# Performance work log

Measured on AMD Instinct MI355X. Metric: run time of the kernel, lower is better.

## Reference

```python
import jax, jax.numpy as jnp
import numpy as np

# (pt, eta, phi) feature indices per particle for each block (eta=None for MET)
A_PT, A_ETA, A_PHI = [5, 4, 35, 34], [9, 8, 45, 44], [13, 12, 55, 54]            # e3,e2,j9,j8
B_PT, B_ETA, B_PHI = [3, 33, 31, 2], [7, 43, 41, 6], [11, 53, 51, 10]            # e1,j7,j5,e0
C_PT, C_ETA, C_PHI = [28, 32, 15, 16], [38, 42, 19, 20], [48, 52, 23, 24]        # j2,j6,mu1,mu2
D_PT, D_ETA, D_PHI = [0, 14, 30, 26, 29, 27, 17], [None, 18, 40, 36, 39, 37, 21], [1, 22, 50, 46, 49, 47, 25]  # MET,mu0,j4,j0,j3,j1,mu3


def _bc(a, nd):
    # broadcast a (B,) or () angle factor over nd trailing qubit axes
    return a.reshape(a.shape + (1,) * nd)


def _rx(state, theta, w):
    nd = state.ndim - 2
    c = _bc(jnp.cos(theta * 0.5), nd)
    s = _bc(jnp.sin(theta * 0.5), nd)
    s0 = jnp.take(state, 0, axis=w + 1)
    s1 = jnp.take(state, 1, axis=w + 1)
    return jnp.stack([c * s0 - 1j * s * s1, -1j * s * s0 + c * s1], axis=w + 1)


def _ry(state, theta, w):
    nd = state.ndim - 2
    c = _bc(jnp.cos(theta * 0.5), nd)
    s = _bc(jnp.sin(theta * 0.5), nd)
    s0 = jnp.take(state, 0, axis=w + 1)
    s1 = jnp.take(state, 1, axis=w + 1)
    return jnp.stack([c * s0 - s * s1, s * s0 + c * s1], axis=w + 1)


def _rz(state, theta, w):
    nd = state.ndim - 2
    ph = _bc(jnp.exp(-0.5j * theta.astype(state.dtype)), nd)
    s0 = jnp.take(state, 0, axis=w + 1)
    s1 = jnp.take(state, 1, axis=w + 1)
    return jnp.stack([ph * s0, jnp.conj(ph) * s1], axis=w + 1)


def _cnot(state, ctrl, tgt):
    c0 = jnp.take(state, 0, axis=ctrl + 1)
    c1 = jnp.take(state, 1, axis=ctrl + 1)
    t_ax = tgt + 1 if tgt < ctrl else tgt  # ctrl axis removed shifts higher wires down
    c1 = jnp.flip(c1, axis=t_ax)
    return jnp.stack([c0, c1], axis=ctrl + 1)


def _extract(x, pt_idx, eta_idx, phi_idx):
    pt = x[:, np.array(pt_idx)]
    eta = jnp.stack([x[:, i] if i is not None else jnp.zeros(x.shape[0], x.dtype) for i in eta_idx], axis=1)
    phi = x[:, np.array(phi_idx)]
    return pt, eta, phi


def _run_block(pt, eta, phi, weights, n, latent, trash, depth):
    B = pt.shape[0]
    state = jnp.zeros((B,) + (2,) * n, dtype=jnp.complex64)
    state = state.at[(slice(None),) + (0,) * n].set(1.0)
    for k in range(n):
        state = _rx(state, eta[:, k], k)
        state = _ry(state, pt[:, k], k)
        state = _rz(state, phi[:, k], k)
    for k in range(n - 1):
        state = _cnot(state, k, k + 1)
    for k in range(n):
        state = _rz(state, eta[:, k], k)
        state = _ry(state, pt[:, k], k)
        state = _rx(state, phi[:, k], k)
    for d in range(depth):
        for t in trash:
            for l in latent:
                state = _cnot(state, t, l)
        for k in range(n):
            state = _ry(state, weights[d * n + k], k)
        for l in latent:
            for t in trash:
                state = _cnot(state, l, t)
    p = jnp.abs(state) ** 2  # (B, 2,...,2) real probabilities
    red = tuple(range(1, n))
    zs = [jnp.sum(jnp.take(p, 0, axis=w + 1), axis=red) - jnp.sum(jnp.take(p, 1, axis=w + 1), axis=red) for w in trash]
    return jnp.stack(zs, axis=1)


def setup_inputs() -> dict:
    key = jax.random.key(0)
    k0, k1, k2, k3, k4 = jax.random.split(key, 5)
    B = 131072
    x = jax.random.normal(k0, (B, 56), dtype=jnp.float32)
    wA = 0.01 * jax.random.normal(k1, (4,), dtype=jnp.float32)
    wB = 0.01 * jax.random.normal(k2, (4,), dtype=jnp.float32)
    wC = 0.01 * jax.random.normal(k3, (4,), dtype=jnp.float32)
    wD = 0.01 * jax.random.normal(k4, (28,), dtype=jnp.float32)
    return {"x": x, "wA": wA, "wB": wB, "wC": wC, "wD": wD}


def reference(x, wA, wB, wC, wD):
    zA = _run_block(*_extract(x, A_PT, A_ETA, A_PHI), wA, 4, (0, 1), (2, 3), 1)  # (B,2)
    zB = _run_block(*_extract(x, B_PT, B_ETA, B_PHI), wB, 4, (0, 1), (2, 3), 1)  # (B,2)
    zC = _run_block(*_extract(x, C_PT, C_ETA, C_PHI), wC, 4, (0, 1), (2, 3), 1)  # (B,2)
    zD = _run_block(*_extract(x, D_PT, D_ETA, D_PHI), wD, 7, (0, 1, 2, 3), (4, 5, 6), 4)  # (B,3)
    return jnp.concatenate([zA, zB, zC, zD], axis=1)  # (B,9) ~ dict values concatenated
```

## Files before the change

kernel.cpp:

```cpp
#include <hip/hip_runtime.h>
#include <hip/hip_fp16.h>


#define DEVINL __device__ __forceinline__

typedef _Float16 hv2 __attribute__((ext_vector_type(2)));
typedef unsigned int u32;
typedef u32 vreg16 __attribute__((ext_vector_type(16)));
typedef u32 vreg64 __attribute__((ext_vector_type(64)));

struct C2 { __half2 rr, mp; };

DEVINL C2 mkc(float re, float im) {
  C2 c; c.rr = __floats2half2_rn(re, re); c.mp = __floats2half2_rn(-im, im); return c;
}
DEVINL __half2 mkamp(float re, float im) { return __floats2half2_rn(re, im); }
DEVINL __half2 swap2(__half2 v) { return __lowhigh2highlow(v); }
DEVINL __half2 cmulc(C2 u, __half2 v) { return __hfma2(u.rr, v, __hmul2(u.mp, swap2(v))); }

DEVINL float ampsq(__half2 v, float acc) {
#if __has_builtin(__builtin_amdgcn_fdot2)
  return __builtin_amdgcn_fdot2(__builtin_bit_cast(hv2, v), __builtin_bit_cast(hv2, v), acc, false);
#else
  float2 f = __half22float2(v);
  return fmaf(f.x, f.x, fmaf(f.y, f.y, acc));
#endif
}

constexpr int parc(int x) { x ^= x >> 4; x ^= x >> 2; x ^= x >> 1; return x & 1; }

struct c32 { float x, y; };
DEVINL c32 cmulf(c32 a, c32 b) { return { a.x*b.x - a.y*b.y, a.x*b.y + a.y*b.x }; }

template<class VT>
DEVINL __half2 vget(const VT& A, int i) { return __builtin_bit_cast(__half2, (u32)A[i]); }
template<class VT>
DEVINL void vset(VT& A, int i, __half2 v) { A[i] = __builtin_bit_cast(u32, v); }

DEVINL __half2 lx1(__half2 v) {
  int q = __shfl_xor(__builtin_bit_cast(int, v), 1, 64);
  return __builtin_bit_cast(__half2, q);
}
DEVINL float lx1f(float v) { return __shfl_xor(v, 1, 64); }


template<int N, int W, class VT>
DEVINL void g_ry(VT& A, __half2 c2, __half2 s2, __half2 ns2) {
  constexpr int M = 1 << (N - 1 - W);
#pragma unroll
  for (int i = 0; i < (1 << N); ++i) if (!(i & M)) {
    const int j = i | M;
    __half2 v0 = vget(A, i), v1 = vget(A, j);
    vset(A, i, __hfma2(c2, v0, __hmul2(ns2, v1)));
    vset(A, j, __hfma2(c2, v1, __hmul2(s2, v0)));
  }
}

template<int N, int W, class VT>
DEVINL void g_u2(VT& A, C2 u00, C2 u01, C2 u10, C2 u11) {
  constexpr int M = 1 << (N - 1 - W);
#pragma unroll
  for (int i = 0; i < (1 << N); ++i) if (!(i & M)) {
    const int j = i | M;
    __half2 v0 = vget(A, i), v1 = vget(A, j), v0s = swap2(v0), v1s = swap2(v1);
    vset(A, i, __hfma2(u00.rr, v0, __hfma2(u00.mp, v0s, __hfma2(u01.rr, v1, __hmul2(u01.mp, v1s)))));
    vset(A, j, __hfma2(u10.rr, v0, __hfma2(u10.mp, v0s, __hfma2(u11.rr, v1, __hmul2(u11.mp, v1s)))));
  }
}

template<int N, int C, int T, class VT>
DEVINL void g_cnot(VT& A) {
  constexpr int CM = 1 << (N - 1 - C), TM = 1 << (N - 1 - T);
#pragma unroll
  for (int i = 0; i < (1 << N); ++i) if ((i & CM) && !(i & TM)) {
    const int j = i | TM;
    __half2 t = vget(A, i); vset(A, i, vget(A, j)); vset(A, j, t);
  }
}

template<int N, int K, class VT>
DEVINL void chain_cnot(VT& A) {
  if constexpr (K < N - 1) { g_cnot<N, K, K + 1>(A); chain_cnot<N, K + 1>(A); }
}


DEVINL void mk_u01(float ce, float se, float cp, float sp, float cf, float sf,
                   c32& u0, c32& u1) {
  u0 = cmulf({cf, -sf}, {cp * ce, sp * se});
  u1 = cmulf({cf,  sf}, {sp * ce, -cp * se});
}

DEVINL void mk_U(float ce, float se, float cp, float sp, float cf, float sf,
                 C2& U00, C2& U01, C2& U10, C2& U11) {
  c32 z = {ce, -se}, zb = {ce, se};
  c32 A = cmulf({cf * cp, -sf * sp}, z);
  c32 T = cmulf({cf * sp,  sf * cp}, zb);
  c32 Cc = cmulf({cf * sp, -sf * cp}, z);
  c32 D = cmulf({cf * cp,  sf * sp}, zb);
  U00 = mkc(A.x, A.y); U01 = mkc(-T.x, -T.y); U10 = mkc(Cc.x, Cc.y); U11 = mkc(D.x, D.y);
}

DEVINL void load_sc(const float* __restrict__ xr, int eta_i, int pt_i, int phi_i,
                    float& ce, float& se, float& cp, float& sp, float& cf, float& sf) {
  float e = (eta_i < 0) ? 0.f : xr[eta_i];
  __sincosf(0.5f * e, &se, &ce);
  __sincosf(0.5f * xr[pt_i], &sp, &cp);
  __sincosf(0.5f * xr[phi_i], &sf, &cf);
}

template<int N, int M, class VT, class CF>
DEVINL void build_rec(VT& A, CF cf) {
  if constexpr (M < N) {
    c32 u0, u1; cf(M, u0, u1);
    C2 c0 = mkc(u0.x, u0.y), c1 = mkc(u1.x, u1.y);
#pragma unroll
    for (int j = (1 << M) - 1; j >= 0; --j) {
      __half2 s = vget(A, j);
      vset(A, 2 * j,     cmulc(c0, s));
      vset(A, 2 * j + 1, cmulc(c1, s));
    }
    build_rec<N, M + 1>(A, cf);
  }
}

template<int N, int K, class VT, class CF>
DEVINL void usweep_rec(VT& A, CF cf) {
  if constexpr (K < N) {
    C2 U00, U01, U10, U11;
    cf(K, U00, U01, U10, U11);
    g_u2<N, K>(A, U00, U01, U10, U11);
    usweep_rec<N, K + 1>(A, cf);
  }
}

template<int N, int K, class VT, class CF>
DEVINL void ry_rec(VT& A, CF cf) {
  if constexpr (K < N) {
    __half2 c2, s2, ns2;
    cf(K, c2, s2, ns2);
    g_ry<N, K>(A, c2, s2, ns2);
    ry_rec<N, K + 1>(A, cf);
  }
}


template<int I>
DEVINL void sim4h(const float* __restrict__ xr, const float* __restrict__ w, float* z) {
  constexpr int PT[3][4]  = {{5, 4, 35, 34}, {3, 33, 31, 2}, {28, 32, 15, 16}};
  constexpr int ETA[3][4] = {{9, 8, 45, 44}, {7, 43, 41, 6}, {38, 42, 19, 20}};
  constexpr int PHI[3][4] = {{13, 12, 55, 54}, {11, 53, 51, 10}, {48, 52, 23, 24}};
  vreg16 A;
  vset(A, 0, mkamp(1.f, 0.f));
  build_rec<4, 0>(A, [&](int M, c32& u0, c32& u1) {
    float ce, se, cp, sp, cf, sf;
    load_sc(xr, ETA[I][M], PT[I][M], PHI[I][M], ce, se, cp, sp, cf, sf);
    mk_u01(ce, se, cp, sp, cf, sf, u0, u1);
  });
  chain_cnot<4, 0>(A);
  usweep_rec<4, 0>(A, [&](int K, C2& U00, C2& U01, C2& U10, C2& U11) {
    float ce, se, cp, sp, cf, sf;
    load_sc(xr, ETA[I][K], PT[I][K], PHI[I][K], ce, se, cp, sp, cf, sf);
    mk_U(ce, se, cp, sp, cf, sf, U00, U01, U10, U11);
  });

#pragma unroll
  for (int i = 0; i < 16; ++i)
    if (parc(i & 3) && !(i & 8)) {
      __half2 t = vget(A, i); vset(A, i, vget(A, i ^ 12)); vset(A, i ^ 12, t);
    }

  ry_rec<4, 0>(A, [&](int K, __half2& c2, __half2& s2, __half2& ns2) {
    float sv, cv; __sincosf(0.5f * w[K], &sv, &cv);
    c2 = __floats2half2_rn(cv, cv);
    s2 = __floats2half2_rn(sv, sv);
    ns2 = __floats2half2_rn(-sv, -sv);
  });

#pragma unroll
  for (int i = 0; i < 16; ++i)
    if (parc(i & 12) && !(i & 2)) {
      __half2 t = vget(A, i); vset(A, i, vget(A, i ^ 3)); vset(A, i ^ 3, t);
    }

  float cls[4];
#pragma unroll
  for (int c = 0; c < 4; ++c) cls[c] = 0.f;
#pragma unroll
  for (int i = 0; i < 16; ++i) cls[i & 3] = ampsq(vget(A, i), cls[i & 3]);
  float z0 = 0.f, z1 = 0.f;
#pragma unroll
  for (int c = 0; c < 4; ++c) {
    z0 += (c & 2) ? -cls[c] : cls[c];
    z1 += (c & 1) ? -cls[c] : cls[c];
  }
  z[0] = z0; z[1] = z1;
}


DEVINL void role7(const float* __restrict__ xr, const float* __restrict__ wD,
                  float* __restrict__ out_row, bool po) {
  constexpr int PT[7]  = {0, 14, 30, 26, 29, 27, 17};
  constexpr int ETA[7] = {-1, 18, 40, 36, 39, 37, 21};
  constexpr int PHI[7] = {1, 22, 50, 46, 49, 47, 25};

  vreg64 A;
  vset(A, 0, mkamp(1.f, 0.f));
  build_rec<6, 0>(A, [&](int M, c32& u0, c32& u1) {
    const int k = M + 1;
    float ce, se, cp, sp, cf, sf;
    load_sc(xr, ETA[k], PT[k], PHI[k], ce, se, cp, sp, cf, sf);
    mk_u01(ce, se, cp, sp, cf, sf, u0, u1);
  });
  {
    float ce, se, cp, sp, cf, sf;
    load_sc(xr, ETA[0], PT[0], PHI[0], ce, se, cp, sp, cf, sf);
    c32 u0, u1; mk_u01(ce, se, cp, sp, cf, sf, u0, u1);
    C2 c0 = mkc(po ? u1.x : u0.x, po ? u1.y : u0.y);
#pragma unroll
    for (int i = 0; i < 64; ++i) vset(A, i, cmulc(c0, vget(A, i)));
  }

#pragma unroll
  for (int i = 0; i < 32; ++i) {
    const int j = i | 32;
    __half2 lo = vget(A, i), hi = vget(A, j);
    vset(A, i, po ? hi : lo);
    vset(A, j, po ? lo : hi);
  }
  chain_cnot<6, 0>(A);

  {
    float ce, se, cp, sp, cf, sf;
    load_sc(xr, ETA[0], PT[0], PHI[0], ce, se, cp, sp, cf, sf);
    C2 U00, U01, U10, U11;
    mk_U(ce, se, cp, sp, cf, sf, U00, U01, U10, U11);
    C2 UA, UB;
    UA.rr = po ? U11.rr : U00.rr; UA.mp = po ? U11.mp : U00.mp;
    UB.rr = po ? U10.rr : U01.rr; UB.mp = po ? U10.mp : U01.mp;
#pragma unroll
    for (int i = 0; i < 64; ++i) {
      __half2 m = vget(A, i), q = lx1(m);
      vset(A, i, __hfma2(UA.rr, m, __hfma2(UA.mp, swap2(m),
                 __hfma2(UB.rr, q, __hmul2(UB.mp, swap2(q))))));
    }
  }
  usweep_rec<6, 0>(A, [&](int W, C2& U00, C2& U01, C2& U10, C2& U11) {
    const int k = W + 1;
    float ce, se, cp, sp, cf, sf;
    load_sc(xr, ETA[k], PT[k], PHI[k], ce, se, cp, sp, cf, sf);
    mk_U(ce, se, cp, sp, cf, sf, U00, U01, U10, U11);
  });

#pragma unroll 1
  for (int d = 0; d < 4; ++d) {
#pragma unroll
    for (int i = 0; i < 64; ++i)
      if (parc(i & 7) && !(i & 0x20)) {
        const int j = i ^ 0x38;
        __half2 t0 = lx1(vget(A, j));
        __half2 t1 = lx1(vget(A, i));
        vset(A, i, t0); vset(A, j, t1);
      }

    {
      float sv, cv; __sincosf(0.5f * wD[7 * d], &sv, &cv);
      __half2 c2v = __floats2half2_rn(cv, cv);
      __half2 sp2 = __floats2half2_rn(po ? sv : -sv, po ? sv : -sv);
#pragma unroll
      for (int i = 0; i < 64; ++i) {
        __half2 q = lx1(vget(A, i));
        vset(A, i, __hfma2(c2v, vget(A, i), __hmul2(sp2, q)));
      }
    }
    ry_rec<6, 0>(A, [&](int W, __half2& c2, __half2& s2, __half2& ns2) {
      float sv, cv; __sincosf(0.5f * wD[7 * d + W + 1], &sv, &cv);
      c2 = __floats2half2_rn(cv, cv);
      s2 = __floats2half2_rn(sv, sv);
      ns2 = __floats2half2_rn(-sv, -sv);
    });

#pragma unroll
    for (int i = 0; i < 64; ++i)
      if (!(i & 4)) {
        const int j = i ^ 7;
        const bool cond = parc(i & 0x38) ? !po : po;
        __half2 lo = vget(A, i), hi = vget(A, j);
        vset(A, i, cond ? hi : lo);
        vset(A, j, cond ? lo : hi);
      }
  }

  float cls[8];
#pragma unroll
  for (int c = 0; c < 8; ++c) cls[c] = 0.f;
#pragma unroll
  for (int i = 0; i < 64; ++i) cls[i & 7] = ampsq(vget(A, i), cls[i & 7]);
  float z4 = 0.f, z5 = 0.f, z6 = 0.f;
#pragma unroll
  for (int c = 0; c < 8; ++c) {
    z4 += (c & 4) ? -cls[c] : cls[c];
    z5 += (c & 2) ? -cls[c] : cls[c];
    z6 += (c & 1) ? -cls[c] : cls[c];
  }
  z4 += lx1f(z4); z5 += lx1f(z5); z6 += lx1f(z6);
  if (!po) {
    out_row[6] = z4; out_row[7] = z5; out_row[8] = z6;
  }
}


__global__ void __launch_bounds__(256, 2)
k_all(const float* __restrict__ x,
      const float* __restrict__ wA, const float* __restrict__ wB,
      const float* __restrict__ wC, const float* __restrict__ wD,
      float* __restrict__ out, int B, int gx) {
  const int bx = blockIdx.x;
  if (bx < gx) {
    const int b = bx * 256 + threadIdx.x;
    if (b >= B) return;
    const float* xr = x + (size_t)b * 56;
    float o[6];
    sim4h<0>(xr, wA, &o[0]);
    sim4h<1>(xr, wB, &o[2]);
    sim4h<2>(xr, wC, &o[4]);
    float* op = out + (size_t)b * 9;
#pragma unroll
    for (int i = 0; i < 6; ++i) op[i] = o[i];
  } else {
    const int t = (bx - gx) * 256 + threadIdx.x;
    const int b = t >> 1;
    if (b >= B) return;
    const bool po = (t & 1) != 0;
    role7(x + (size_t)b * 56, wD, out + (size_t)b * 9, po);
  }
}


extern "C" void kernel_launch(void* const* d_in, const int* in_sizes, int n_in,
                              void* d_out, int out_size, void* d_ws, size_t ws_size,
                              hipStream_t stream) {
  const float* x  = (const float*)d_in[0];
  const float* wA = (const float*)d_in[1];
  const float* wB = (const float*)d_in[2];
  const float* wC = (const float*)d_in[3];
  const float* wD = (const float*)d_in[4];
  float* out = (float*)d_out;
  const int B = in_sizes[0] / 56;
  const int threads = 256;

  const int gx = (B + threads - 1) / threads;
  const int gy = (2 * B + threads - 1) / threads;
  k_all<<<gx + gy, threads, 0, stream>>>(x, wA, wB, wC, wD, out, B, gx);
}
```

Measured before the change: 138.4 us.

## Split 7-qubit block state across four lanes instead of two

The 7-qubit simulation now distributes the 128-amplitude state over four lanes (32 half2 registers each) rather than two lanes with 64 registers. Gates on the top two qubits become cross-lane shuffles with xor 1, 2 or 3, and the CNOT permutations are rewritten for the new lane mapping. The launch-bounds occupancy hint rises from 2 to 8 to use the lower register pressure. The cost is twice as many threads for this block, more shuffles per gate, redundant per-lane angle computation, and an extra shuffle-reduction step at the end.

```diff
diff --git a/kernel.cpp b/kernel.cpp
--- a/kernel.cpp
+++ b/kernel.cpp
@@ -7,7 +7,7 @@
 typedef _Float16 hv2 __attribute__((ext_vector_type(2)));
 typedef unsigned int u32;
 typedef u32 vreg16 __attribute__((ext_vector_type(16)));
-typedef u32 vreg64 __attribute__((ext_vector_type(64)));
+typedef u32 vreg32 __attribute__((ext_vector_type(32)));
 
 struct C2 { __half2 rr, mp; };
 
@@ -37,11 +37,13 @@
 template<class VT>
 DEVINL void vset(VT& A, int i, __half2 v) { A[i] = __builtin_bit_cast(u32, v); }
 
-DEVINL __half2 lx1(__half2 v) {
-  int q = __shfl_xor(__builtin_bit_cast(int, v), 1, 64);
+template<int K>
+DEVINL __half2 lxk(__half2 v) {
+  int q = __shfl_xor(__builtin_bit_cast(int, v), K, 64);
   return __builtin_bit_cast(__half2, q);
 }
-DEVINL float lx1f(float v) { return __shfl_xor(v, 1, 64); }
+template<int K>
+DEVINL float lxkf(float v) { return __shfl_xor(v, K, 64); }
 
 
 template<int N, int W, class VT>
@@ -198,15 +200,18 @@
 
 
 DEVINL void role7(const float* __restrict__ xr, const float* __restrict__ wD,
-                  float* __restrict__ out_row, bool po) {
+                  float* __restrict__ out_row, int sub) {
+  const bool b0 = (sub & 2) != 0;
+  const bool b1 = (sub & 1) != 0;
+
   constexpr int PT[7]  = {0, 14, 30, 26, 29, 27, 17};
   constexpr int ETA[7] = {-1, 18, 40, 36, 39, 37, 21};
   constexpr int PHI[7] = {1, 22, 50, 46, 49, 47, 25};
 
-  vreg64 A;
+  vreg32 A;
   vset(A, 0, mkamp(1.f, 0.f));
-  build_rec<6, 0>(A, [&](int M, c32& u0, c32& u1) {
-    const int k = M + 1;
+  build_rec<5, 0>(A, [&](int M, c32& u0, c32& u1) {
+    const int k = M + 2;
     float ce, se, cp, sp, cf, sf;
     load_sc(xr, ETA[k], PT[k], PHI[k], ce, se, cp, sp, cf, sf);
     mk_u01(ce, se, cp, sp, cf, sf, u0, u1);
@@ -214,20 +219,30 @@
   {
     float ce, se, cp, sp, cf, sf;
     load_sc(xr, ETA[0], PT[0], PHI[0], ce, se, cp, sp, cf, sf);
-    c32 u0, u1; mk_u01(ce, se, cp, sp, cf, sf, u0, u1);
-    C2 c0 = mkc(po ? u1.x : u0.x, po ? u1.y : u0.y);
-#pragma unroll
-    for (int i = 0; i < 64; ++i) vset(A, i, cmulc(c0, vget(A, i)));
+    c32 q0u0, q0u1; mk_u01(ce, se, cp, sp, cf, sf, q0u0, q0u1);
+    load_sc(xr, ETA[1], PT[1], PHI[1], ce, se, cp, sp, cf, sf);
+    c32 q1u0, q1u1; mk_u01(ce, se, cp, sp, cf, sf, q1u0, q1u1);
+    c32 f0 = b0 ? q0u1 : q0u0;
+    c32 f1 = b1 ? q1u1 : q1u0;
+    c32 f = cmulf(f0, f1);
+    C2 cf2 = mkc(f.x, f.y);
+#pragma unroll
+    for (int i = 0; i < 32; ++i) vset(A, i, cmulc(cf2, vget(A, i)));
   }
 
 #pragma unroll
   for (int i = 0; i < 32; ++i) {
-    const int j = i | 32;
+    __half2 q = lxk<1>(vget(A, i));
+    if (true) vset(A, i, b0 ? q : vget(A, i));
+  }
+#pragma unroll
+  for (int i = 0; i < 16; ++i) {
+    const int j = i | 16;
     __half2 lo = vget(A, i), hi = vget(A, j);
-    vset(A, i, po ? hi : lo);
-    vset(A, j, po ? lo : hi);
-  }
-  chain_cnot<6, 0>(A);
+    vset(A, i, b1 ? hi : lo);
+    vset(A, j, b1 ? lo : hi);
+  }
+  chain_cnot<5, 0>(A);
 
   {
     float ce, se, cp, sp, cf, sf;
@@ -235,17 +250,32 @@
     C2 U00, U01, U10, U11;
     mk_U(ce, se, cp, sp, cf, sf, U00, U01, U10, U11);
     C2 UA, UB;
-    UA.rr = po ? U11.rr : U00.rr; UA.mp = po ? U11.mp : U00.mp;
-    UB.rr = po ? U10.rr : U01.rr; UB.mp = po ? U10.mp : U01.mp;
-#pragma unroll
-    for (int i = 0; i < 64; ++i) {
-      __half2 m = vget(A, i), q = lx1(m);
+    UA.rr = b0 ? U11.rr : U00.rr; UA.mp = b0 ? U11.mp : U00.mp;
+    UB.rr = b0 ? U10.rr : U01.rr; UB.mp = b0 ? U10.mp : U01.mp;
+#pragma unroll
+    for (int i = 0; i < 32; ++i) {
+      __half2 m = vget(A, i), q = lxk<2>(m);
       vset(A, i, __hfma2(UA.rr, m, __hfma2(UA.mp, swap2(m),
                  __hfma2(UB.rr, q, __hmul2(UB.mp, swap2(q))))));
     }
   }
-  usweep_rec<6, 0>(A, [&](int W, C2& U00, C2& U01, C2& U10, C2& U11) {
-    const int k = W + 1;
+  {
+    float ce, se, cp, sp, cf, sf;
+    load_sc(xr, ETA[1], PT[1], PHI[1], ce, se, cp, sp, cf, sf);
+    C2 U00, U01, U10, U11;
+    mk_U(ce, se, cp, sp, cf, sf, U00, U01, U10, U11);
+    C2 UA, UB;
+    UA.rr = b1 ? U11.rr : U00.rr; UA.mp = b1 ? U11.mp : U00.mp;
+    UB.rr = b1 ? U10.rr : U01.rr; UB.mp = b1 ? U10.mp : U01.mp;
+#pragma unroll
+    for (int i = 0; i < 32; ++i) {
+      __half2 m = vget(A, i), q = lxk<1>(m);
+      vset(A, i, __hfma2(UA.rr, m, __hfma2(UA.mp, swap2(m),
+                 __hfma2(UB.rr, q, __hmul2(UB.mp, swap2(q))))));
+    }
+  }
+  usweep_rec<5, 0>(A, [&](int W, C2& U00, C2& U01, C2& U10, C2& U11) {
+    const int k = W + 2;
     float ce, se, cp, sp, cf, sf;
     load_sc(xr, ETA[k], PT[k], PHI[k], ce, se, cp, sp, cf, sf);
     mk_U(ce, se, cp, sp, cf, sf, U00, U01, U10, U11);
@@ -254,47 +284,60 @@
 #pragma unroll 1
   for (int d = 0; d < 4; ++d) {
 #pragma unroll
-    for (int i = 0; i < 64; ++i)
-      if (parc(i & 7) && !(i & 0x20)) {
-        const int j = i ^ 0x38;
-        __half2 t0 = lx1(vget(A, j));
-        __half2 t1 = lx1(vget(A, i));
+    for (int i = 0; i < 32; ++i)
+      if (parc(i & 7) && !(i & 0x10)) {
+        const int j = i ^ 0x18;
+        __half2 t0 = lxk<3>(vget(A, j));
+        __half2 t1 = lxk<3>(vget(A, i));
         vset(A, i, t0); vset(A, j, t1);
       }
 
     {
       float sv, cv; __sincosf(0.5f * wD[7 * d], &sv, &cv);
       __half2 c2v = __floats2half2_rn(cv, cv);
-      __half2 sp2 = __floats2half2_rn(po ? sv : -sv, po ? sv : -sv);
-#pragma unroll
-      for (int i = 0; i < 64; ++i) {
-        __half2 q = lx1(vget(A, i));
-        vset(A, i, __hfma2(c2v, vget(A, i), __hmul2(sp2, q)));
+      __half2 se2 = __floats2half2_rn(b0 ? sv : -sv, b0 ? sv : -sv);
+#pragma unroll
+      for (int i = 0; i < 32; ++i) {
+        __half2 q = lxk<2>(vget(A, i));
+        vset(A, i, __hfma2(c2v, vget(A, i), __hmul2(se2, q)));
       }
     }
-    ry_rec<6, 0>(A, [&](int W, __half2& c2, __half2& s2, __half2& ns2) {
-      float sv, cv; __sincosf(0.5f * wD[7 * d + W + 1], &sv, &cv);
+    {
+      float sv, cv; __sincosf(0.5f * wD[7 * d + 1], &sv, &cv);
+      __half2 c2v = __floats2half2_rn(cv, cv);
+      __half2 se2 = __floats2half2_rn(b1 ? sv : -sv, b1 ? sv : -sv);
+#pragma unroll
+      for (int i = 0; i < 32; ++i) {
+        __half2 q = lxk<1>(vget(A, i));
+        vset(A, i, __hfma2(c2v, vget(A, i), __hmul2(se2, q)));
+      }
+    }
+    ry_rec<5, 0>(A, [&](int W, __half2& c2, __half2& s2, __half2& ns2) {
+      float sv, cv; __sincosf(0.5f * wD[7 * d + W + 2], &sv, &cv);
       c2 = __floats2half2_rn(cv, cv);
       s2 = __floats2half2_rn(sv, sv);
       ns2 = __floats2half2_rn(-sv, -sv);
     });
 
-#pragma unroll
-    for (int i = 0; i < 64; ++i)
-      if (!(i & 4)) {
-        const int j = i ^ 7;
-        const bool cond = parc(i & 0x38) ? !po : po;
-        __half2 lo = vget(A, i), hi = vget(A, j);
-        vset(A, i, cond ? hi : lo);
-        vset(A, j, cond ? lo : hi);
-      }
+    {
+      const bool ps = b0 ^ b1;
+#pragma unroll
+      for (int i = 0; i < 32; ++i)
+        if (!(i & 4)) {
+          const int j = i ^ 7;
+          const bool cond = parc(i & 0x18) ? !ps : ps;
+          __half2 lo = vget(A, i), hi = vget(A, j);
+          vset(A, i, cond ? hi : lo);
+          vset(A, j, cond ? lo : hi);
+        }
+    }
   }
 
   float cls[8];
 #pragma unroll
   for (int c = 0; c < 8; ++c) cls[c] = 0.f;
 #pragma unroll
-  for (int i = 0; i < 64; ++i) cls[i & 7] = ampsq(vget(A, i), cls[i & 7]);
+  for (int i = 0; i < 32; ++i) cls[i & 7] = ampsq(vget(A, i), cls[i & 7]);
   float z4 = 0.f, z5 = 0.f, z6 = 0.f;
 #pragma unroll
   for (int c = 0; c < 8; ++c) {
@@ -302,14 +345,15 @@
     z5 += (c & 2) ? -cls[c] : cls[c];
     z6 += (c & 1) ? -cls[c] : cls[c];
   }
-  z4 += lx1f(z4); z5 += lx1f(z5); z6 += lx1f(z6);
-  if (!po) {
+  z4 += lxkf<1>(z4); z5 += lxkf<1>(z5); z6 += lxkf<1>(z6);
+  z4 += lxkf<2>(z4); z5 += lxkf<2>(z5); z6 += lxkf<2>(z6);
+  if (sub == 0) {
     out_row[6] = z4; out_row[7] = z5; out_row[8] = z6;
   }
 }
 
 
-__global__ void __launch_bounds__(256, 2)
+__global__ void __launch_bounds__(256, 8)
 k_all(const float* __restrict__ x,
       const float* __restrict__ wA, const float* __restrict__ wB,
       const float* __restrict__ wC, const float* __restrict__ wD,
@@ -328,10 +372,9 @@
     for (int i = 0; i < 6; ++i) op[i] = o[i];
   } else {
     const int t = (bx - gx) * 256 + threadIdx.x;
-    const int b = t >> 1;
+    const int b = t >> 2;
     if (b >= B) return;
-    const bool po = (t & 1) != 0;
-    role7(x + (size_t)b * 56, wD, out + (size_t)b * 9, po);
+    role7(x + (size_t)b * 56, wD, out + (size_t)b * 9, t & 3);
   }
 }
 
@@ -349,6 +392,6 @@
   const int threads = 256;
 
   const int gx = (B + threads - 1) / threads;
-  const int gy = (2 * B + threads - 1) / threads;
+  const int gy = (4 * B + threads - 1) / threads;
   k_all<<<gx + gy, threads, 0, stream>>>(x, wA, wB, wC, wD, out, B, gx);
 }
```

New measurement: 186.3 us. 1.35x slower.

## Simulate 7-qubit block fully per thread with 128-entry register state

Applied to the files above, without the earlier changes.

Replaces the two-lanes-per-sample split of the 7-qubit circuit, which used cross-lane shuffles, with a single thread holding all 128 half2 amplitudes in two 64-register vectors. All four blocks are now computed by one thread per sample in a single uniform grid, removing lane shuffles, the po-dependent selects and the separate block role. The cost is doubled register pressure per thread (128 state registers) under launch_bounds(256,2), which risks spills or lower occupancy, and fewer threads in flight overall.

```diff
diff --git a/kernel.cpp b/kernel.cpp
--- a/kernel.cpp
+++ b/kernel.cpp
@@ -37,11 +37,15 @@
 template<class VT>
 DEVINL void vset(VT& A, int i, __half2 v) { A[i] = __builtin_bit_cast(u32, v); }
 
-DEVINL __half2 lx1(__half2 v) {
-  int q = __shfl_xor(__builtin_bit_cast(int, v), 1, 64);
-  return __builtin_bit_cast(__half2, q);
-}
-DEVINL float lx1f(float v) { return __shfl_xor(v, 1, 64); }
+struct S128 { vreg64 lo, hi; };
+DEVINL __half2 vget(const S128& A, int i) {
+  u32 u = (i < 64) ? (u32)A.lo[i] : (u32)A.hi[i - 64];
+  return __builtin_bit_cast(__half2, u);
+}
+DEVINL void vset(S128& A, int i, __half2 v) {
+  u32 u = __builtin_bit_cast(u32, v);
+  if (i < 64) A.lo[i] = u; else A.hi[i - 64] = u;
+}
 
 
 template<int N, int W, class VT>
@@ -197,96 +201,45 @@
 }
 
 
-DEVINL void role7(const float* __restrict__ xr, const float* __restrict__ wD,
-                  float* __restrict__ out_row, bool po) {
+DEVINL void sim7(const float* __restrict__ xr, const float* __restrict__ wD,
+                 float* z) {
   constexpr int PT[7]  = {0, 14, 30, 26, 29, 27, 17};
   constexpr int ETA[7] = {-1, 18, 40, 36, 39, 37, 21};
   constexpr int PHI[7] = {1, 22, 50, 46, 49, 47, 25};
 
-  vreg64 A;
+  S128 A;
   vset(A, 0, mkamp(1.f, 0.f));
-  build_rec<6, 0>(A, [&](int M, c32& u0, c32& u1) {
-    const int k = M + 1;
-    float ce, se, cp, sp, cf, sf;
-    load_sc(xr, ETA[k], PT[k], PHI[k], ce, se, cp, sp, cf, sf);
+  build_rec<7, 0>(A, [&](int M, c32& u0, c32& u1) {
+    float ce, se, cp, sp, cf, sf;
+    load_sc(xr, ETA[M], PT[M], PHI[M], ce, se, cp, sp, cf, sf);
     mk_u01(ce, se, cp, sp, cf, sf, u0, u1);
   });
-  {
-    float ce, se, cp, sp, cf, sf;
-    load_sc(xr, ETA[0], PT[0], PHI[0], ce, se, cp, sp, cf, sf);
-    c32 u0, u1; mk_u01(ce, se, cp, sp, cf, sf, u0, u1);
-    C2 c0 = mkc(po ? u1.x : u0.x, po ? u1.y : u0.y);
-#pragma unroll
-    for (int i = 0; i < 64; ++i) vset(A, i, cmulc(c0, vget(A, i)));
-  }
-
-#pragma unroll
-  for (int i = 0; i < 32; ++i) {
-    const int j = i | 32;
-    __half2 lo = vget(A, i), hi = vget(A, j);
-    vset(A, i, po ? hi : lo);
-    vset(A, j, po ? lo : hi);
-  }
-  chain_cnot<6, 0>(A);
-
-  {
-    float ce, se, cp, sp, cf, sf;
-    load_sc(xr, ETA[0], PT[0], PHI[0], ce, se, cp, sp, cf, sf);
-    C2 U00, U01, U10, U11;
-    mk_U(ce, se, cp, sp, cf, sf, U00, U01, U10, U11);
-    C2 UA, UB;
-    UA.rr = po ? U11.rr : U00.rr; UA.mp = po ? U11.mp : U00.mp;
-    UB.rr = po ? U10.rr : U01.rr; UB.mp = po ? U10.mp : U01.mp;
-#pragma unroll
-    for (int i = 0; i < 64; ++i) {
-      __half2 m = vget(A, i), q = lx1(m);
-      vset(A, i, __hfma2(UA.rr, m, __hfma2(UA.mp, swap2(m),
-                 __hfma2(UB.rr, q, __hmul2(UB.mp, swap2(q))))));
-    }
-  }
-  usweep_rec<6, 0>(A, [&](int W, C2& U00, C2& U01, C2& U10, C2& U11) {
-    const int k = W + 1;
-    float ce, se, cp, sp, cf, sf;
-    load_sc(xr, ETA[k], PT[k], PHI[k], ce, se, cp, sp, cf, sf);
+  chain_cnot<7, 0>(A);
+  usweep_rec<7, 0>(A, [&](int K, C2& U00, C2& U01, C2& U10, C2& U11) {
+    float ce, se, cp, sp, cf, sf;
+    load_sc(xr, ETA[K], PT[K], PHI[K], ce, se, cp, sp, cf, sf);
     mk_U(ce, se, cp, sp, cf, sf, U00, U01, U10, U11);
   });
 
 #pragma unroll 1
   for (int d = 0; d < 4; ++d) {
 #pragma unroll
-    for (int i = 0; i < 64; ++i)
-      if (parc(i & 7) && !(i & 0x20)) {
-        const int j = i ^ 0x38;
-        __half2 t0 = lx1(vget(A, j));
-        __half2 t1 = lx1(vget(A, i));
-        vset(A, i, t0); vset(A, j, t1);
+    for (int i = 0; i < 128; ++i)
+      if (parc(i & 7) && !(i & 64)) {
+        __half2 t = vget(A, i); vset(A, i, vget(A, i ^ 0x78)); vset(A, i ^ 0x78, t);
       }
 
-    {
-      float sv, cv; __sincosf(0.5f * wD[7 * d], &sv, &cv);
-      __half2 c2v = __floats2half2_rn(cv, cv);
-      __half2 sp2 = __floats2half2_rn(po ? sv : -sv, po ? sv : -sv);
-#pragma unroll
-      for (int i = 0; i < 64; ++i) {
-        __half2 q = lx1(vget(A, i));
-        vset(A, i, __hfma2(c2v, vget(A, i), __hmul2(sp2, q)));
-      }
-    }
-    ry_rec<6, 0>(A, [&](int W, __half2& c2, __half2& s2, __half2& ns2) {
-      float sv, cv; __sincosf(0.5f * wD[7 * d + W + 1], &sv, &cv);
+    ry_rec<7, 0>(A, [&](int K, __half2& c2, __half2& s2, __half2& ns2) {
+      float sv, cv; __sincosf(0.5f * wD[7 * d + K], &sv, &cv);
       c2 = __floats2half2_rn(cv, cv);
       s2 = __floats2half2_rn(sv, sv);
       ns2 = __floats2half2_rn(-sv, -sv);
     });
 
 #pragma unroll
-    for (int i = 0; i < 64; ++i)
-      if (!(i & 4)) {
-        const int j = i ^ 7;
-        const bool cond = parc(i & 0x38) ? !po : po;
-        __half2 lo = vget(A, i), hi = vget(A, j);
-        vset(A, i, cond ? hi : lo);
-        vset(A, j, cond ? lo : hi);
+    for (int i = 0; i < 128; ++i)
+      if (parc(i & 0x78) && !(i & 4)) {
+        __half2 t = vget(A, i); vset(A, i, vget(A, i ^ 7)); vset(A, i ^ 7, t);
       }
   }
 
@@ -294,7 +247,7 @@
 #pragma unroll
   for (int c = 0; c < 8; ++c) cls[c] = 0.f;
 #pragma unroll
-  for (int i = 0; i < 64; ++i) cls[i & 7] = ampsq(vget(A, i), cls[i & 7]);
+  for (int i = 0; i < 128; ++i) cls[i & 7] = ampsq(vget(A, i), cls[i & 7]);
   float z4 = 0.f, z5 = 0.f, z6 = 0.f;
 #pragma unroll
   for (int c = 0; c < 8; ++c) {
@@ -302,10 +255,7 @@
     z5 += (c & 2) ? -cls[c] : cls[c];
     z6 += (c & 1) ? -cls[c] : cls[c];
   }
-  z4 += lx1f(z4); z5 += lx1f(z5); z6 += lx1f(z6);
-  if (!po) {
-    out_row[6] = z4; out_row[7] = z5; out_row[8] = z6;
-  }
+  z[0] = z4; z[1] = z5; z[2] = z6;
 }
 
 
@@ -313,26 +263,20 @@
 k_all(const float* __restrict__ x,
       const float* __restrict__ wA, const float* __restrict__ wB,
       const float* __restrict__ wC, const float* __restrict__ wD,
-      float* __restrict__ out, int B, int gx) {
-  const int bx = blockIdx.x;
-  if (bx < gx) {
-    const int b = bx * 256 + threadIdx.x;
-    if (b >= B) return;
-    const float* xr = x + (size_t)b * 56;
-    float o[6];
-    sim4h<0>(xr, wA, &o[0]);
-    sim4h<1>(xr, wB, &o[2]);
-    sim4h<2>(xr, wC, &o[4]);
-    float* op = out + (size_t)b * 9;
-#pragma unroll
-    for (int i = 0; i < 6; ++i) op[i] = o[i];
-  } else {
-    const int t = (bx - gx) * 256 + threadIdx.x;
-    const int b = t >> 1;
-    if (b >= B) return;
-    const bool po = (t & 1) != 0;
-    role7(x + (size_t)b * 56, wD, out + (size_t)b * 9, po);
-  }
+      float* __restrict__ out, int B) {
+  const int b = blockIdx.x * 256 + threadIdx.x;
+  if (b >= B) return;
+  const float* xr = x + (size_t)b * 56;
+
+  float o[9];
+  sim4h<0>(xr, wA, &o[0]);
+  sim4h<1>(xr, wB, &o[2]);
+  sim4h<2>(xr, wC, &o[4]);
+  sim7(xr, wD, &o[6]);
+
+  float* op = out + (size_t)b * 9;
+#pragma unroll
+  for (int i = 0; i < 9; ++i) op[i] = o[i];
 }
 
 
@@ -348,7 +292,6 @@
   const int B = in_sizes[0] / 56;
   const int threads = 256;
 
-  const int gx = (B + threads - 1) / threads;
-  const int gy = (2 * B + threads - 1) / threads;
-  k_all<<<gx + gy, threads, 0, stream>>>(x, wA, wB, wC, wD, out, B, gx);
-}
+  const int blocks = (B + threads - 1) / threads;
+  k_all<<<blocks, threads, 0, stream>>>(x, wA, wB, wC, wD, out, B);
+}
```

Measured after the change: 129.3 us, median of 2. 1.07x faster.
